# Kernel optimization log

Hardware: AMD Instinct MI355X
Metric: run time of the kernel (lower is better)

The kernel has to match this reference:

```python
import jax, jax.numpy as jnp
import numpy as np

N_NODES = 100000
BN_EPS = 1e-5


def gcn_conv(x, src, dst, W, b, n):
    # PyG GCNConv: add self-loops, symmetric norm D^-1/2 (A+I) D^-1/2, then linear.
    h = x @ W                                   # [N, F_out]
    deg = jnp.zeros((n,), h.dtype).at[dst].add(1.0)   # in-degree incl. self-loops
    dinv = jnp.where(deg > 0, jax.lax.rsqrt(deg), 0.0)
    norm = dinv[src] * dinv[dst]                # [E+N]
    msg = h[src] * norm[:, None]                # gather + scale, [E+N, F_out]
    out = jax.ops.segment_sum(msg, dst, num_segments=n)
    return out + b


def setup_inputs() -> dict:
    key = jax.random.key(0)
    ks = jax.random.split(key, 6)
    N, E, F_in, H, C = N_NODES, 1600000, 128, 64, 64
    x = jax.random.normal(ks[0], (N, F_in), dtype=jnp.float32)
    edge_index = jax.random.randint(ks[1], (2, E), 0, N, dtype=jnp.int64)
    W1 = jax.random.normal(ks[2], (F_in, H), dtype=jnp.float32) * (1.0 / np.sqrt(F_in))
    b1 = jnp.zeros((H,), jnp.float32)
    W2 = jax.random.normal(ks[3], (H, C), dtype=jnp.float32) * (1.0 / np.sqrt(H))
    b2 = jnp.zeros((C,), jnp.float32)
    gamma = jnp.ones((H,), jnp.float32)
    beta = jnp.zeros((H,), jnp.float32)
    return {"x": x, "edge_index": edge_index, "W1": W1, "b1": b1,
            "W2": W2, "b2": b2, "gamma": gamma, "beta": beta}


def reference(x, edge_index, W1, b1, W2, b2, gamma, beta):
    n = x.shape[0]
    loop = jnp.arange(n, dtype=edge_index.dtype)
    src = jnp.concatenate([edge_index[0], loop])
    dst = jnp.concatenate([edge_index[1], loop])
    # dropout(p=0.8) acts as identity in eval mode (deterministic baseline)
    h = gcn_conv(x, src, dst, W1, b1, n)
    # BatchNorm1d with batch statistics (biased var), as in training-mode math
    mean = jnp.mean(h, axis=0)
    var = jnp.mean(jnp.square(h - mean), axis=0)
    h = (h - mean) * jax.lax.rsqrt(var + BN_EPS) * gamma + beta
    h = jax.nn.relu(h)
    out = gcn_conv(h, src, dst, W2, b2, n)
    return out
```

## Files before the change

### kernel.cpp

```cpp
#include <hip/hip_runtime.h>

#define BN_EPS 1e-5f
#define SCAN_CHUNK 2048
#define EPB 16384
#define NBUCK 512

__device__ __forceinline__ float bf2f(unsigned short u) {
  return __uint_as_float(((unsigned)u) << 16);
}
__device__ __forceinline__ unsigned short f2bf(float f) {
  unsigned b = __float_as_uint(f);
  b += 0x7FFFu + ((b >> 16) & 1u);
  return (unsigned short)(b >> 16);
}

template<int K, bool FUSE_BN, bool SCALE>
__device__ __forceinline__ void gemm_tile(float* __restrict__ Xs,
                                          float* __restrict__ bn_s, int tile,
                                          const float* __restrict__ X,
                                          const float* __restrict__ W,
                                          const float* __restrict__ dinv,
                                          const float* __restrict__ stats,
                                          const float* __restrict__ gamma,
                                          const float* __restrict__ beta,
                                          unsigned short* __restrict__ Y,
                                          int n, float inv_n) {
  constexpr int XS = K + 4;
  const int t = threadIdx.x;
  const int base = tile * 64;
  float* mean_s = bn_s;
  float* scl_s  = bn_s + 64;
  float* bt_s   = bn_s + 128;

  if (FUSE_BN) {
    if (t < 64) {
      float mean = stats[t] * inv_n;
      float var = stats[64 + t] * inv_n - mean * mean;
      mean_s[t] = mean;
      scl_s[t] = rsqrtf(var + BN_EPS) * gamma[t];
      bt_s[t] = beta[t];
    }
    __syncthreads();
  }

  {
    constexpr int RV = K / 4;
    for (int idx = t; idx < 64 * RV; idx += 256) {
      int row = idx / RV, kk = idx % RV;
      float4 v = make_float4(0.f, 0.f, 0.f, 0.f);
      if (base + row < n) {
        v = *(const float4*)(X + (size_t)(base + row) * K + kk * 4);
        if (FUSE_BN) {
          int k0 = kk * 4;
          v.x = fmaxf(fmaf(v.x - mean_s[k0 + 0], scl_s[k0 + 0], bt_s[k0 + 0]), 0.f);
          v.y = fmaxf(fmaf(v.y - mean_s[k0 + 1], scl_s[k0 + 1], bt_s[k0 + 1]), 0.f);
          v.z = fmaxf(fmaf(v.z - mean_s[k0 + 2], scl_s[k0 + 2], bt_s[k0 + 2]), 0.f);
          v.w = fmaxf(fmaf(v.w - mean_s[k0 + 3], scl_s[k0 + 3], bt_s[k0 + 3]), 0.f);
        }
      }
      *(float4*)(Xs + row * XS + kk * 4) = v;
    }
  }
  __syncthreads();

  const int tc = t & 15;
  const int tr = t >> 4;
  const float* wp = W + tc * 4;

  float acc[4][4];
#pragma unroll
  for (int r = 0; r < 4; ++r)
#pragma unroll
    for (int c = 0; c < 4; ++c) acc[r][c] = 0.f;

  float4 wc[4], wn[4];
#pragma unroll
  for (int kk = 0; kk < 4; ++kk) wc[kk] = *(const float4*)(wp + kk * 64);

#pragma unroll 4
  for (int k = 0; k < K; k += 4) {
    float4 xr[4];
#pragma unroll
    for (int r = 0; r < 4; ++r) xr[r] = *(const float4*)(Xs + (tr * 4 + r) * XS + k);
    if (k + 4 < K) {
#pragma unroll
      for (int kk = 0; kk < 4; ++kk) wn[kk] = *(const float4*)(wp + (k + 4 + kk) * 64);
    }
#pragma unroll
    for (int kk = 0; kk < 4; ++kk) {
#pragma unroll
      for (int r = 0; r < 4; ++r) {
        float xv = (kk == 0) ? xr[r].x : (kk == 1) ? xr[r].y : (kk == 2) ? xr[r].z : xr[r].w;
        acc[r][0] = fmaf(xv, wc[kk].x, acc[r][0]);
        acc[r][1] = fmaf(xv, wc[kk].y, acc[r][1]);
        acc[r][2] = fmaf(xv, wc[kk].z, acc[r][2]);
        acc[r][3] = fmaf(xv, wc[kk].w, acc[r][3]);
      }
    }
    if (k + 4 < K) {
#pragma unroll
      for (int kk = 0; kk < 4; ++kk) wc[kk] = wn[kk];
    }
  }

#pragma unroll
  for (int r = 0; r < 4; ++r) {
    int i = base + tr * 4 + r;
    if (i < n) {
      float sc = SCALE ? dinv[i] : 1.0f;
      ushort4 o;
      o.x = f2bf(acc[r][0] * sc);
      o.y = f2bf(acc[r][1] * sc);
      o.z = f2bf(acc[r][2] * sc);
      o.w = f2bf(acc[r][3] * sc);
      *(ushort4*)(Y + (size_t)i * 64 + tc * 4) = o;
    }
  }
}

__global__ __launch_bounds__(256) void k_fused_hist_gemm1(
    const int* __restrict__ dst, int* __restrict__ bh, int E, int nba,
    const float* __restrict__ X, const float* __restrict__ W,
    unsigned short* __restrict__ Y, int n, int nbT) {
  __shared__ float Xs[64 * 132];

  int paired = 2 * (nba < nbT ? nba : nbT);
  int role, idx;
  if ((int)blockIdx.x < paired) {
    role = blockIdx.x & 1;
    idx = blockIdx.x >> 1;
  } else {
    int r = blockIdx.x - paired;
    if (nba > nbT) { role = 0; idx = nbT + r; }
    else           { role = 1; idx = nba + r; }
  }

  if (role == 0) {
    int* hist = (int*)Xs;
    const int t = threadIdx.x;
    for (int b = t; b < NBUCK; b += 256) hist[b] = 0;
    __syncthreads();
    int ebase = idx * EPB;
#pragma unroll
    for (int i = 0; i < EPB / 1024; ++i) {
      int e = ebase + (i * 256 + t) * 4;
      if (e + 3 < E) {
        int4 d4 = *(const int4*)(dst + e);
        atomicAdd(&hist[d4.x >> 8], 1);
        atomicAdd(&hist[d4.y >> 8], 1);
        atomicAdd(&hist[d4.z >> 8], 1);
        atomicAdd(&hist[d4.w >> 8], 1);
      } else {
        for (int q = e; q < E && q < e + 4; ++q) atomicAdd(&hist[dst[q] >> 8], 1);
      }
    }
    __syncthreads();
    for (int b = t; b < NBUCK; b += 256) bh[(size_t)b * nba + idx] = hist[b];
    return;
  }
  gemm_tile<128, false, false>(Xs, nullptr, idx, X, W,
                               nullptr, nullptr, nullptr, nullptr, Y, n, 0.f);
}

__global__ __launch_bounds__(256) void k_bscan_local(int* __restrict__ a,
                                                     int* __restrict__ bsum, int M) {
  __shared__ int ts[256];
  int base = blockIdx.x * SCAN_CHUNK;
  int t = threadIdx.x;
  int idx0 = base + t * 8;
  int v[8];
  int s = 0;
#pragma unroll
  for (int k = 0; k < 8; ++k) {
    int i = idx0 + k;
    int d = (i < M) ? a[i] : 0;
    v[k] = s;
    s += d;
  }
  int val = s;
  ts[t] = val;
  __syncthreads();
#pragma unroll
  for (int off = 1; off < 256; off <<= 1) {
    int add = (t >= off) ? ts[t - off] : 0;
    __syncthreads();
    val += add;
    ts[t] = val;
    __syncthreads();
  }
  int excl = val - s;
#pragma unroll
  for (int k = 0; k < 8; ++k) {
    int i = idx0 + k;
    if (i < M) a[i] = excl + v[k];
  }
  if (t == 255) bsum[blockIdx.x] = val;
}

__global__ void k_bscan_blk(int* __restrict__ bsum, int nblk) {
  if (threadIdx.x == 0) {
    int run = 0;
    for (int i = 0; i < nblk; ++i) { int v = bsum[i]; bsum[i] = run; run += v; }
  }
}

__global__ __launch_bounds__(256) void k_bscan_add(int* __restrict__ a,
                                                   const int* __restrict__ bsum, int M) {
  int off = bsum[blockIdx.x];
  int base = blockIdx.x * SCAN_CHUNK;
  for (int k = threadIdx.x; k < SCAN_CHUNK; k += 256) {
    int i = base + k;
    if (i < M) a[i] += off;
  }
}

__global__ __launch_bounds__(256) void k_scatter(
    const int* __restrict__ src, const int* __restrict__ dst,
    const int* __restrict__ bh, int* __restrict__ sval, int E, int nba) {
  __shared__ int cur[NBUCK];
  const int t = threadIdx.x;
  for (int b = t; b < NBUCK; b += 256) cur[b] = bh[(size_t)b * nba + blockIdx.x];
  __syncthreads();
  int ebase = blockIdx.x * EPB;
#pragma unroll
  for (int i = 0; i < EPB / 1024; ++i) {
    int e = ebase + (i * 256 + t) * 4;
    if (e + 3 < E) {
      int4 d4 = *(const int4*)(dst + e);
      int4 s4 = *(const int4*)(src + e);
      int p0 = atomicAdd(&cur[d4.x >> 8], 1);
      int p1 = atomicAdd(&cur[d4.y >> 8], 1);
      int p2 = atomicAdd(&cur[d4.z >> 8], 1);
      int p3 = atomicAdd(&cur[d4.w >> 8], 1);
      sval[p0] = s4.x | ((d4.x & 255) << 20);
      sval[p1] = s4.y | ((d4.y & 255) << 20);
      sval[p2] = s4.z | ((d4.z & 255) << 20);
      sval[p3] = s4.w | ((d4.w & 255) << 20);
    } else {
      for (int q = e; q < E && q < e + 4; ++q) {
        int d = dst[q];
        int p = atomicAdd(&cur[d >> 8], 1);
        sval[p] = src[q] | ((d & 255) << 20);
      }
    }
  }
}

__global__ __launch_bounds__(256) void k_group_deg(
    const int* __restrict__ sval, const int* __restrict__ bh,
    int* __restrict__ deg, int nba, int n) {
  __shared__ int cnt[256];
  const int t = threadIdx.x;
  const int b = blockIdx.x;
  cnt[t] = 0;
  __syncthreads();
  int lo = bh[(size_t)b * nba];
  int end = bh[(size_t)(b + 1) * nba];
  for (int i = lo + t; i < end; i += 256)
    atomicAdd(&cnt[(sval[i] >> 20) & 255], 1);
  __syncthreads();
  int node = b * 256 + t;
  if (node < n) deg[node] = cnt[t];
}


__global__ __launch_bounds__(256) void k_scan_local(const int* __restrict__ deg,
                                                    int* __restrict__ row_ptr,
                                                    int* __restrict__ blksum,
                                                    float* __restrict__ dinv, int n) {
  __shared__ int ts[256];
  int base = blockIdx.x * SCAN_CHUNK;
  int t = threadIdx.x;
  int idx0 = base + t * 8;
  int v[8];
  int s = 0;
#pragma unroll
  for (int k = 0; k < 8; ++k) {
    int i = idx0 + k;
    int d = (i < n) ? deg[i] : 0;
    if (i < n) dinv[i] = rsqrtf(1.0f + (float)d);
    v[k] = s;
    s += d;
  }
  int val = s;
  ts[t] = val;
  __syncthreads();
#pragma unroll
  for (int off = 1; off < 256; off <<= 1) {
    int add = (t >= off) ? ts[t - off] : 0;
    __syncthreads();
    val += add;
    ts[t] = val;
    __syncthreads();
  }
  int excl = val - s;
#pragma unroll
  for (int k = 0; k < 8; ++k) {
    int i = idx0 + k;
    if (i < n) row_ptr[i] = excl + v[k];
  }
  if (t == 255) blksum[blockIdx.x] = val;
}

__global__ void k_scan_blk(int* __restrict__ blksum, int nblk,
                           int* __restrict__ row_ptr, int n,
                           float* __restrict__ stats) {
  for (int i = threadIdx.x; i < 128; i += 64) stats[i] = 0.f;
  if (threadIdx.x == 0) {
    int run = 0;
    for (int i = 0; i < nblk; ++i) { int v = blksum[i]; blksum[i] = run; run += v; }
    row_ptr[n] = run;
  }
}

__global__ __launch_bounds__(256) void k_scan_add(int* __restrict__ row_ptr,
                                                  const int* __restrict__ blksum, int n) {
  int off = blksum[blockIdx.x];
  int base = blockIdx.x * SCAN_CHUNK;
  for (int k = threadIdx.x; k < SCAN_CHUNK; k += 256) {
    int i = base + k;
    if (i < n) row_ptr[i] += off;
  }
}

__global__ __launch_bounds__(256) void k_fused_fill_scale(
    const int* __restrict__ sval, const int* __restrict__ bh,
    const int* __restrict__ row_ptr, int* __restrict__ col, int nba, int nbu,
    unsigned short* __restrict__ h16, const float* __restrict__ dinv, int n) {
  __shared__ int cur[256];
  const int t = threadIdx.x;
  if ((int)blockIdx.x < nbu) {
    const int b = blockIdx.x;
    int node = b * 256 + t;
    cur[t] = (node < n) ? row_ptr[node] : 0;
    __syncthreads();
    int lo = bh[(size_t)b * nba];
    int end = bh[(size_t)(b + 1) * nba];
    for (int i = lo + t; i < end; i += 256) {
      int v = sval[i];
      int p = atomicAdd(&cur[(v >> 20) & 255], 1);
      col[p] = v & 0x1FFFF;
    }
    return;
  }
  int si = blockIdx.x - nbu;
  int idx = (si * 256 + t) * 8;
  if (idx >= n * 64) return;
  int row = idx >> 6;
  float di = dinv[row];
  uint4 v = *(const uint4*)(h16 + idx);
  unsigned r[4] = {v.x, v.y, v.z, v.w};
#pragma unroll
  for (int q = 0; q < 4; ++q) {
    float lo = bf2f((unsigned short)(r[q] & 0xFFFFu)) * di;
    float hi = bf2f((unsigned short)(r[q] >> 16)) * di;
    r[q] = ((unsigned)f2bf(hi) << 16) | f2bf(lo);
  }
  *(uint4*)(h16 + idx) = make_uint4(r[0], r[1], r[2], r[3]);
}

__global__ __launch_bounds__(256) void k_gather_pair(
    const unsigned short* __restrict__ Hs,
    const int* __restrict__ row_ptr,
    const int* __restrict__ col,
    const float* __restrict__ dinv,
    const float* __restrict__ b,
    float* __restrict__ out, int n) {
  const unsigned* H32 = (const unsigned*)Hs;
  int lane = threadIdx.x & 63;
  int wv = threadIdx.x >> 6;
  int i = blockIdx.x * 4 + wv;
  if (i >= n) return;
  int half = lane >> 5;
  int q = lane & 31;
  int p0 = row_ptr[i], p1 = row_ptr[i + 1];
  int L = (p1 - p0) + 1;
  float a0 = 0.f, a1 = 0.f;
  int k = half;
  for (; k + 6 < L; k += 8) {
    int c0 = (k == 0) ? i : col[p0 + k - 1];
    int c1 = col[p0 + k + 1];
    int c2 = col[p0 + k + 3];
    int c3 = col[p0 + k + 5];
    unsigned w0 = H32[(size_t)c0 * 32 + q];
    unsigned w1 = H32[(size_t)c1 * 32 + q];
    unsigned w2 = H32[(size_t)c2 * 32 + q];
    unsigned w3 = H32[(size_t)c3 * 32 + q];
    a0 += bf2f((unsigned short)(w0 & 0xFFFFu)) + bf2f((unsigned short)(w1 & 0xFFFFu))
        + bf2f((unsigned short)(w2 & 0xFFFFu)) + bf2f((unsigned short)(w3 & 0xFFFFu));
    a1 += bf2f((unsigned short)(w0 >> 16)) + bf2f((unsigned short)(w1 >> 16))
        + bf2f((unsigned short)(w2 >> 16)) + bf2f((unsigned short)(w3 >> 16));
  }
  for (; k < L; k += 2) {
    int c = (k == 0) ? i : col[p0 + k - 1];
    unsigned w = H32[(size_t)c * 32 + q];
    a0 += bf2f((unsigned short)(w & 0xFFFFu));
    a1 += bf2f((unsigned short)(w >> 16));
  }
  a0 += __shfl_down(a0, 32);
  a1 += __shfl_down(a1, 32);
  if (lane < 32) {
    float di = dinv[i];
    float2 bb = *(const float2*)(b + 2 * q);
    float2 o;
    o.x = fmaf(di, a0, bb.x);
    o.y = fmaf(di, a1, bb.y);
    *(float2*)(out + (size_t)i * 64 + 2 * q) = o;
  }
}

__global__ __launch_bounds__(256) void k_bnstats(const float* __restrict__ A,
                                                 float* __restrict__ stats, int n) {
  int j = threadIdx.x & 63;
  int r = threadIdx.x >> 6;
  float s = 0.f, s2 = 0.f;
  for (int i = blockIdx.x * 4 + r; i < n; i += gridDim.x * 4) {
    float v = A[(size_t)i * 64 + j];
    s += v;
    s2 += v * v;
  }
  __shared__ float ls[256], ls2[256];
  ls[threadIdx.x] = s;
  ls2[threadIdx.x] = s2;
  __syncthreads();
  if (threadIdx.x < 64) {
    atomicAdd(&stats[j], ls[j] + ls[j + 64] + ls[j + 128] + ls[j + 192]);
    atomicAdd(&stats[64 + j], ls2[j] + ls2[j + 64] + ls2[j + 128] + ls2[j + 192]);
  }
}

__global__ __launch_bounds__(256) void k_gemm2(const float* __restrict__ X,
                                               const float* __restrict__ W,
                                               const float* __restrict__ dinv,
                                               const float* __restrict__ stats,
                                               const float* __restrict__ gamma,
                                               const float* __restrict__ beta,
                                               unsigned short* __restrict__ Y,
                                               int n, float inv_n) {
  __shared__ float Xs[64 * 68];
  __shared__ float bn_s[192];
  gemm_tile<64, true, true>(Xs, bn_s, blockIdx.x, X, W, dinv, stats, gamma, beta,
                            Y, n, inv_n);
}


extern "C" void kernel_launch(void* const* d_in, const int* in_sizes, int n_in,
                              void* d_out, int out_size, void* d_ws, size_t ws_size,
                              hipStream_t stream) {
  const float* x     = (const float*)d_in[0];
  const int*   ei    = (const int*)d_in[1];
  const float* W1    = (const float*)d_in[2];
  const float* b1    = (const float*)d_in[3];
  const float* W2    = (const float*)d_in[4];
  const float* b2    = (const float*)d_in[5];
  const float* gamma = (const float*)d_in[6];
  const float* beta  = (const float*)d_in[7];
  float* out = (float*)d_out;

  const int N = in_sizes[0] / 128;
  const int E = in_sizes[1] / 2;
  const int* src = ei;
  const int* dst = ei + E;

  const size_t Npad = ((size_t)N + 256) & ~(size_t)255;

  char* p = (char*)d_ws;
  float* dinv    = (float*)p;               p += Npad * 4;
  int*   deg     = (int*)p;                 p += Npad * 4;
  int*   row_ptr = (int*)p;                 p += Npad * 4;
  int*   blksum  = (int*)p;                 p += 256 * 4;
  int*   sval    = (int*)p;                 p += (size_t)E * 4;
  int*   col     = (int*)p;                 p += (size_t)E * 4;
  unsigned short* h16 = (unsigned short*)p; p += (size_t)N * 64 * 2;
  float* agg     = (float*)p;               p += (size_t)N * 64 * 4;
  float* stats   = (float*)p;               p += 128 * 4;

  int* bh = (int*)agg;

  int nb_n4 = (N + 3) / 4;
  int nb_t  = (N + 63) / 64;
  int nba   = (E + EPB - 1) / EPB;
  int nbu   = (N + 255) / 256;
  int nbS   = (N * 64 + 2047) / 2048;
  int nscan = (N + SCAN_CHUNK - 1) / SCAN_CHUNK;
  int M     = NBUCK * nba;
  int nbM   = (M + SCAN_CHUNK - 1) / SCAN_CHUNK;
  float inv_n = 1.0f / (float)N;

  k_fused_hist_gemm1<<<nba + nb_t, 256, 0, stream>>>(dst, bh, E, nba,
                                                     x, W1, h16, N, nb_t);

  k_bscan_local<<<nbM, 256, 0, stream>>>(bh, blksum, M);
  k_bscan_blk<<<1, 64, 0, stream>>>(blksum, nbM);
  k_bscan_add<<<nbM, 256, 0, stream>>>(bh, blksum, M);
  k_scatter<<<nba, 256, 0, stream>>>(src, dst, bh, sval, E, nba);

  k_group_deg<<<nbu, 256, 0, stream>>>(sval, bh, deg, nba, N);

  k_scan_local<<<nscan, 256, 0, stream>>>(deg, row_ptr, blksum, dinv, N);
  k_scan_blk<<<1, 64, 0, stream>>>(blksum, nscan, row_ptr, N, stats);
  k_scan_add<<<nscan, 256, 0, stream>>>(row_ptr, blksum, N);

  k_fused_fill_scale<<<nbu + nbS, 256, 0, stream>>>(sval, bh, row_ptr, col,
                                                    nba, nbu, h16, dinv, N);

  k_gather_pair<<<nb_n4, 256, 0, stream>>>(h16, row_ptr, col, dinv, b1, agg, N);

  k_bnstats<<<1024, 256, 0, stream>>>(agg, stats, N);

  k_gemm2<<<nb_t, 256, 0, stream>>>(agg, W2, dinv, stats, gamma, beta, h16, N, inv_n);
  k_gather_pair<<<nb_n4, 256, 0, stream>>>(h16, row_ptr, col, dinv, b2, out, N);
}
```

Measured before the change: 387.9 us.

## Gather neighbors in quarter-wave groups with wave-preloaded column indices

The SpMM gather kernel now splits each 64-lane wave into four 16-lane groups, each loading 8-byte (4 bf16) chunks per neighbor row, so four neighbors are processed concurrently instead of two. The first 64 column indices are loaded once, cooperatively, into lanes and broadcast with shuffles, removing the serial dependent col[] loads from the inner loop. Rows with more than 63 neighbors fall back to a strided loop, and the final reduction adds one extra shuffle stage. The tail uses predicated FMA with a zero weight, which adds a little wasted load traffic on short rows.

```diff
diff --git a/kernel.cpp b/kernel.cpp
--- a/kernel.cpp
+++ b/kernel.cpp
@@ -359,53 +359,73 @@
   *(uint4*)(h16 + idx) = make_uint4(r[0], r[1], r[2], r[3]);
 }
 
-__global__ __launch_bounds__(256) void k_gather_pair(
+__global__ __launch_bounds__(256) void k_gather_quad(
     const unsigned short* __restrict__ Hs,
     const int* __restrict__ row_ptr,
     const int* __restrict__ col,
     const float* __restrict__ dinv,
     const float* __restrict__ b,
     float* __restrict__ out, int n) {
-  const unsigned* H32 = (const unsigned*)Hs;
+  const uint2* H64 = (const uint2*)Hs;
   int lane = threadIdx.x & 63;
   int wv = threadIdx.x >> 6;
   int i = blockIdx.x * 4 + wv;
   if (i >= n) return;
-  int half = lane >> 5;
-  int q = lane & 31;
+  int quarter = lane >> 4;
+  int q = lane & 15;
   int p0 = row_ptr[i], p1 = row_ptr[i + 1];
-  int L = (p1 - p0) + 1;
-  float a0 = 0.f, a1 = 0.f;
-  int k = half;
-  for (; k + 6 < L; k += 8) {
-    int c0 = (k == 0) ? i : col[p0 + k - 1];
-    int c1 = col[p0 + k + 1];
-    int c2 = col[p0 + k + 3];
-    int c3 = col[p0 + k + 5];
-    unsigned w0 = H32[(size_t)c0 * 32 + q];
-    unsigned w1 = H32[(size_t)c1 * 32 + q];
-    unsigned w2 = H32[(size_t)c2 * 32 + q];
-    unsigned w3 = H32[(size_t)c3 * 32 + q];
-    a0 += bf2f((unsigned short)(w0 & 0xFFFFu)) + bf2f((unsigned short)(w1 & 0xFFFFu))
-        + bf2f((unsigned short)(w2 & 0xFFFFu)) + bf2f((unsigned short)(w3 & 0xFFFFu));
-    a1 += bf2f((unsigned short)(w0 >> 16)) + bf2f((unsigned short)(w1 >> 16))
-        + bf2f((unsigned short)(w2 >> 16)) + bf2f((unsigned short)(w3 >> 16));
-  }
-  for (; k < L; k += 2) {
-    int c = (k == 0) ? i : col[p0 + k - 1];
-    unsigned w = H32[(size_t)c * 32 + q];
-    a0 += bf2f((unsigned short)(w & 0xFFFFu));
-    a1 += bf2f((unsigned short)(w >> 16));
-  }
-  a0 += __shfl_down(a0, 32);
-  a1 += __shfl_down(a1, 32);
-  if (lane < 32) {
+  int nl = p1 - p0;
+  int L = nl + 1;
+  int cl = (lane == 0) ? i : ((lane <= nl) ? col[p0 + lane - 1] : i);
+  float a0 = 0.f, a1 = 0.f, a2 = 0.f, a3 = 0.f;
+  int Lc = (L < 64) ? L : 64;
+  int k = 0;
+  for (; k + 16 <= Lc; k += 16) {
+#pragma unroll
+    for (int j = 0; j < 4; ++j) {
+      int c = __shfl(cl, k + quarter * 4 + j);
+      uint2 u = H64[(size_t)c * 16 + q];
+      a0 += bf2f((unsigned short)u.x);
+      a1 += bf2f((unsigned short)(u.x >> 16));
+      a2 += bf2f((unsigned short)u.y);
+      a3 += bf2f((unsigned short)(u.y >> 16));
+    }
+  }
+  if (k < Lc) {
+#pragma unroll
+    for (int j = 0; j < 4; ++j) {
+      int vidx = k + quarter * 4 + j;
+      int vc = (vidx < Lc) ? vidx : (Lc - 1);
+      int c = __shfl(cl, vc);
+      uint2 u = H64[(size_t)c * 16 + q];
+      float w = (vidx < Lc) ? 1.0f : 0.0f;
+      a0 = fmaf(w, bf2f((unsigned short)u.x), a0);
+      a1 = fmaf(w, bf2f((unsigned short)(u.x >> 16)), a1);
+      a2 = fmaf(w, bf2f((unsigned short)u.y), a2);
+      a3 = fmaf(w, bf2f((unsigned short)(u.y >> 16)), a3);
+    }
+  }
+  for (int v = 64 + quarter; v < L; v += 4) {
+    int c = col[p0 + v - 1];
+    uint2 u = H64[(size_t)c * 16 + q];
+    a0 += bf2f((unsigned short)u.x);
+    a1 += bf2f((unsigned short)(u.x >> 16));
+    a2 += bf2f((unsigned short)u.y);
+    a3 += bf2f((unsigned short)(u.y >> 16));
+  }
+  a0 += __shfl_down(a0, 16); a0 += __shfl_down(a0, 32);
+  a1 += __shfl_down(a1, 16); a1 += __shfl_down(a1, 32);
+  a2 += __shfl_down(a2, 16); a2 += __shfl_down(a2, 32);
+  a3 += __shfl_down(a3, 16); a3 += __shfl_down(a3, 32);
+  if (lane < 16) {
     float di = dinv[i];
-    float2 bb = *(const float2*)(b + 2 * q);
-    float2 o;
+    float4 bb = *(const float4*)(b + 4 * q);
+    float4 o;
     o.x = fmaf(di, a0, bb.x);
     o.y = fmaf(di, a1, bb.y);
-    *(float2*)(out + (size_t)i * 64 + 2 * q) = o;
+    o.z = fmaf(di, a2, bb.z);
+    o.w = fmaf(di, a3, bb.w);
+    *(float4*)(out + (size_t)i * 64 + 4 * q) = o;
   }
 }
 
@@ -504,10 +524,10 @@
   k_fused_fill_scale<<<nbu + nbS, 256, 0, stream>>>(sval, bh, row_ptr, col,
                                                     nba, nbu, h16, dinv, N);
 
-  k_gather_pair<<<nb_n4, 256, 0, stream>>>(h16, row_ptr, col, dinv, b1, agg, N);
+  k_gather_quad<<<nb_n4, 256, 0, stream>>>(h16, row_ptr, col, dinv, b1, agg, N);
 
   k_bnstats<<<1024, 256, 0, stream>>>(agg, stats, N);
 
   k_gemm2<<<nb_t, 256, 0, stream>>>(agg, W2, dinv, stats, gamma, beta, h16, N, inv_n);
-  k_gather_pair<<<nb_n4, 256, 0, stream>>>(h16, row_ptr, col, dinv, b2, out, N);
-}
+  k_gather_quad<<<nb_n4, 256, 0, stream>>>(h16, row_ptr, col, dinv, b2, out, N);
+}
```

Result: faster. 340.5 us (-12.2%).
